# Kernel tuning notes

Measured on AMD Instinct MI355X. Metric: run time of the kernel, lower is better.

## Reference

```python
import jax, jax.numpy as jnp
import numpy as np

N_NODES = 51200
N_GRAPHS = 64
NODES_PER_GRAPH = 800
N_EDGES = 819200
DIM_IN = 128
DIM_HIDDEN = 64
HEADS = 3
DIM_OUT = 64


def leaky(x, slope):
    return jnp.where(x >= 0, x, slope * x)


def setup_inputs() -> dict:
    key = jax.random.key(0)
    ks = jax.random.split(key, 12)
    s = lambda fan_in: 1.0 / np.sqrt(fan_in)
    X = jax.random.normal(ks[0], (N_NODES, DIM_IN), dtype=jnp.float32)
    edge_indices = jax.random.randint(ks[1], (2, N_EDGES), 0, N_NODES, dtype=jnp.int32)
    ptr = (jnp.arange(N_GRAPHS + 1, dtype=jnp.int32) * NODES_PER_GRAPH)
    # linearSeq: Linear(dim_in, dim_hidden) + LeakyReLU
    W1 = jax.random.uniform(ks[2], (DIM_IN, DIM_HIDDEN), jnp.float32, -s(DIM_IN), s(DIM_IN))
    b1 = jax.random.uniform(ks[3], (DIM_HIDDEN,), jnp.float32, -s(DIM_IN), s(DIM_IN))
    # GATConv params: lin_src/lin_dst (no bias), att_src/att_dst, bias (concat=False -> out_channels)
    W_src = jax.random.uniform(ks[4], (DIM_HIDDEN, HEADS * DIM_HIDDEN), jnp.float32, -s(DIM_HIDDEN), s(DIM_HIDDEN))
    W_dst = jax.random.uniform(ks[5], (DIM_HIDDEN, HEADS * DIM_HIDDEN), jnp.float32, -s(DIM_HIDDEN), s(DIM_HIDDEN))
    att_src = jax.random.normal(ks[6], (HEADS, DIM_HIDDEN), dtype=jnp.float32) * 0.1
    att_dst = jax.random.normal(ks[7], (HEADS, DIM_HIDDEN), dtype=jnp.float32) * 0.1
    gat_bias = jnp.zeros((DIM_HIDDEN,), dtype=jnp.float32)
    # linear_final: Linear(2*dim_hidden, dim_out)
    Wf = jax.random.uniform(ks[8], (2 * DIM_HIDDEN, DIM_OUT), jnp.float32, -s(2 * DIM_HIDDEN), s(2 * DIM_HIDDEN))
    bf = jax.random.uniform(ks[9], (DIM_OUT,), jnp.float32, -s(2 * DIM_HIDDEN), s(2 * DIM_HIDDEN))
    return {"X": X, "W1": W1, "b1": b1, "W_src": W_src, "W_dst": W_dst,
            "att_src": att_src, "att_dst": att_dst, "gat_bias": gat_bias,
            "Wf": Wf, "bf": bf, "edge_indices": edge_indices, "ptr": ptr}


def reference(X, W1, b1, W_src, W_dst, att_src, att_dst, gat_bias, Wf, bf, edge_indices, ptr):
    N = X.shape[0]
    src, dst = edge_indices[0], edge_indices[1]  # message flows src -> dst
    # input projection
    h = leaky(X @ W1 + b1, 0.01)                                  # [N, DH]
    # GATConv (heads=3, concat=False, add_self_loops=False)
    x_src = (h @ W_src).reshape(N, HEADS, DIM_HIDDEN)             # [N, H, C]
    x_dst = (h @ W_dst).reshape(N, HEADS, DIM_HIDDEN)
    a_src = jnp.einsum('nhc,hc->nh', x_src, att_src)              # [N, H]
    a_dst = jnp.einsum('nhc,hc->nh', x_dst, att_dst)
    logits = leaky(a_src[src] + a_dst[dst], 0.2)                  # [E, H]
    # segment softmax over incoming edges of each target node
    m = jax.ops.segment_max(logits, dst, num_segments=N)          # [N, H]
    e = jnp.exp(logits - m[dst])
    denom = jax.ops.segment_sum(e, dst, num_segments=N)           # [N, H]
    attn = e / denom[dst]                                         # [E, H]
    msg = x_src[src] * attn[..., None]                            # [E, H, C]
    agg = jax.ops.segment_sum(msg, dst, num_segments=N)           # [N, H, C]
    out = agg.mean(axis=1) + gat_bias                             # concat=False -> head mean
    # final head
    cat = jnp.concatenate([h, out], axis=1)                       # [N, 2*DH]
    y = leaky(cat, 0.01) @ Wf + bf                                # [N, DO]
    # aggregate_using_ptr: mean-pool nodes per graph using CSR ptr
    node_graph = jnp.searchsorted(ptr, jnp.arange(N), side='right') - 1
    sums = jax.ops.segment_sum(y, node_graph, num_segments=ptr.shape[0] - 1)
    counts = (ptr[1:] - ptr[:-1]).astype(y.dtype)
    pooled = sums / counts[:, None]                               # [n_graphs, DO]
    return pooled, attn
```

## Files before the change

kernel.cpp:

```cpp
#include <hip/hip_runtime.h>
#include <hip/hip_bf16.h>

#define N_NODES   51200
#define N_GRAPHS  64
#define N_EDGES   819200
#define DIM_IN    128
#define DH        64
#define HEADS     3
#define DIM_OUT   64
#define CAP       96
#define NPART     8
#define PART_SZ   (N_NODES / NPART)

typedef __hip_bfloat16 bf16;
typedef short bf16x8 __attribute__((ext_vector_type(8)));
typedef float f32x4  __attribute__((ext_vector_type(4)));
typedef float f32x2  __attribute__((ext_vector_type(2)));

__device__ __forceinline__ float b2f(bf16 x) { return __bfloat162float(x); }
__device__ __forceinline__ bf16  f2b(float x) { return __float2bfloat16(x); }
__device__ __forceinline__ short f2bs(float x) { return (short)__bfloat16_as_ushort(f2b(x)); }
__device__ __forceinline__ float leaky(float x, float s) { return x >= 0.f ? x : s * x; }
__device__ __forceinline__ float ldin(const void* p, size_t i, int f32) {
    return f32 ? ((const float*)p)[i] : b2f(((const bf16*)p)[i]);
}
__device__ __forceinline__ bf16x8 ld8(const void* p, size_t i, int f32) {
    if (!f32) return *((const bf16x8*)((const short*)p + i));
    const float* f = (const float*)p + i;
    bf16x8 r;
    #pragma unroll
    for (int j = 0; j < 8; ++j) r[j] = f2bs(f[j]);
    return r;
}

__global__ __launch_bounds__(256) void detect_kernel(const unsigned short* __restrict__ Xu,
                                                     int* __restrict__ flag) {
    __shared__ int cnt;
    int tid = threadIdx.x;
    if (tid == 0) cnt = 0;
    __syncthreads();
    int local = 0;
    for (int i = tid * 2; i < 8192; i += 512) {
        unsigned e = (Xu[i] >> 7) & 0xFF;
        if (e >= 110 && e <= 135) local++;
    }
    atomicAdd(&cnt, local);
    __syncthreads();
    if (tid == 0) *flag = (cnt < 2048) ? 1 : 0;
}

__global__ __launch_bounds__(256) void scatter_prep_kernel(const int* __restrict__ src,
                                                           const int* __restrict__ dst,
                                                           int* __restrict__ cursor,
                                                           unsigned short* __restrict__ bucket,
                                                           const void* __restrict__ W1,
                                                           const void* __restrict__ Wsrc,
                                                           const void* __restrict__ Wdst,
                                                           const void* __restrict__ Wf,
                                                           const void* __restrict__ att_src,
                                                           const void* __restrict__ att_dst,
                                                           const int* __restrict__ flagp,
                                                           short* __restrict__ W1t,
                                                           short* __restrict__ Wallt,
                                                           short* __restrict__ Wft,
                                                           short* __restrict__ Wat) {
    if (blockIdx.x < NPART * (N_EDGES / 2048)) {
        const int p = blockIdx.x & (NPART - 1);
        const int slice = blockIdx.x >> 3;
        const int lo = p * PART_SZ, hi = lo + PART_SZ;
        const int base = slice * 2048 + threadIdx.x;
        #pragma unroll
        for (int t = 0; t < 8; ++t) {
            int e = base + t * 256;
            int d = dst[e];
            if (d >= lo && d < hi) {
                int pos = atomicAdd(&cursor[d], 1);
                if (pos < CAP) bucket[(size_t)d * CAP + pos] = (unsigned short)src[e];
            }
        }
        return;
    }
    const int f32 = *flagp;
    int idx = (blockIdx.x - NPART * (N_EDGES / 2048)) * 256 + threadIdx.x;
    if (idx < 8192) {
        int n = idx >> 7, k = idx & 127;
        W1t[idx] = f2bs(ldin(W1, (size_t)k * 64 + n, f32));
    } else if (idx < 8192 + 12288) {
        int j = idx - 8192;
        int n = j >> 6, k = j & 63;
        Wallt[j] = f2bs(ldin(Wsrc, (size_t)k * 192 + n, f32));
    } else if (idx < 8192 + 12288 + 8192) {
        int j = idx - 20480;
        int n = j >> 7, k = j & 127;
        Wft[j] = f2bs(ldin(Wf, (size_t)k * 64 + n, f32));
    } else if (idx < 8192 + 12288 + 8192 + 1024) {
        int j = idx - 28672;
        int n = j >> 6, k = j & 63;
        float v = 0.f;
        if (n < 3) {
            for (int c = 0; c < 64; ++c)
                v += ldin(Wsrc, (size_t)k * 192 + n * 64 + c, f32) * ldin(att_src, n * 64 + c, f32);
        } else if (n < 6) {
            for (int c = 0; c < 64; ++c)
                v += ldin(Wdst, (size_t)k * 192 + (n - 3) * 64 + c, f32) * ldin(att_dst, (n - 3) * 64 + c, f32);
        }
        Wat[j] = f2bs(v);
    }
}

__global__ __launch_bounds__(64) void k1_kernel(const void* __restrict__ X,
                                                const short* __restrict__ W1t,
                                                const short* __restrict__ Wallt,
                                                const short* __restrict__ Wat,
                                                const void* __restrict__ b1,
                                                const int* __restrict__ flagp,
                                                bf16* __restrict__ h_bf,
                                                unsigned* __restrict__ x8,
                                                float* __restrict__ a_src4,
                                                float* __restrict__ a_dst4) {
    const int f32 = *flagp;
    __shared__ short hs[16 * 72];
    const int lane = threadIdx.x & 63;
    const int lm   = lane & 15;
    const int q    = lane >> 4;
    const int row0 = blockIdx.x * 16;

    #pragma unroll
    for (int ct = 0; ct < 4; ++ct) {
        f32x4 acc = {0.f, 0.f, 0.f, 0.f};
        #pragma unroll
        for (int kc = 0; kc < 4; ++kc) {
            bf16x8 a = ld8(X, (size_t)(row0 + lm) * 128 + kc * 32 + q * 8, f32);
            bf16x8 b = *((const bf16x8*)(W1t + (size_t)(ct * 16 + lm) * 128 + kc * 32 + q * 8));
            acc = __builtin_amdgcn_mfma_f32_16x16x32_bf16(a, b, acc, 0, 0, 0);
        }
        const float bias = ldin(b1, ct * 16 + lm, f32);
        #pragma unroll
        for (int r = 0; r < 4; ++r) {
            int rl = q * 4 + r;
            float v = leaky(acc[r] + bias, 0.01f);
            short hv = f2bs(v);
            hs[rl * 72 + ct * 16 + lm] = hv;
            h_bf[(size_t)(row0 + rl) * 64 + ct * 16 + lm] = __ushort_as_bfloat16((unsigned short)hv);
        }
    }
    asm volatile("s_waitcnt lgkmcnt(0)" ::: "memory");

    bf16x8 a0 = *((const bf16x8*)(hs + lm * 72 + q * 8));
    bf16x8 a1 = *((const bf16x8*)(hs + lm * 72 + 32 + q * 8));
    #pragma unroll
    for (int t = 0; t < 4; ++t) {
        f32x4 acc[3];
        #pragma unroll
        for (int hh = 0; hh < 3; ++hh) {
            acc[hh] = (f32x4){0.f, 0.f, 0.f, 0.f};
            bf16x8 b0 = *((const bf16x8*)(Wallt + (size_t)(hh * 64 + t * 16 + lm) * 64 + q * 8));
            bf16x8 b1v = *((const bf16x8*)(Wallt + (size_t)(hh * 64 + t * 16 + lm) * 64 + 32 + q * 8));
            acc[hh] = __builtin_amdgcn_mfma_f32_16x16x32_bf16(a0, b0, acc[hh], 0, 0, 0);
            acc[hh] = __builtin_amdgcn_mfma_f32_16x16x32_bf16(a1, b1v, acc[hh], 0, 0, 0);
        }
        #pragma unroll
        for (int r = 0; r < 4; ++r) {
            int row = row0 + q * 4 + r;
            unsigned p = (unsigned)__builtin_amdgcn_cvt_pk_fp8_f32(acc[0][r], acc[1][r], 0, false);
            p = (unsigned)__builtin_amdgcn_cvt_pk_fp8_f32(acc[2][r], 0.f, (int)p, true);
            x8[(size_t)row * 64 + t * 16 + lm] = p;
        }
    }
    f32x4 acca = {0.f, 0.f, 0.f, 0.f};
    bf16x8 b0 = *((const bf16x8*)(Wat + (size_t)lm * 64 + q * 8));
    bf16x8 b1v = *((const bf16x8*)(Wat + (size_t)lm * 64 + 32 + q * 8));
    acca = __builtin_amdgcn_mfma_f32_16x16x32_bf16(a0, b0, acca, 0, 0, 0);
    acca = __builtin_amdgcn_mfma_f32_16x16x32_bf16(a1, b1v, acca, 0, 0, 0);
    if (lm < 6) {
        #pragma unroll
        for (int r = 0; r < 4; ++r) {
            int row = row0 + q * 4 + r;
            if (lm < 3) a_src4[(size_t)row * 4 + lm] = acca[r];
            else        a_dst4[(size_t)row * 4 + (lm - 3)] = acca[r];
        }
    }
}

__global__ __launch_bounds__(256) void edge_kernel(const unsigned short* __restrict__ bucket,
                                                   const int* __restrict__ cursor,
                                                   const float* __restrict__ a_src4,
                                                   const float* __restrict__ a_dst4,
                                                   const unsigned* __restrict__ x8,
                                                   const void* __restrict__ gat_bias,
                                                   const int* __restrict__ flagp,
                                                   float4* __restrict__ dstinfo,
                                                   bf16* __restrict__ out_agg) {
    const int f32 = *flagp;
    const int lane = threadIdx.x & 63;
    const int w = threadIdx.x >> 6;
    const int n = blockIdx.x * 4 + w;
    const int dg = min(cursor[n], CAP);
    const float4 ad = ((const float4*)a_dst4)[n];
    __shared__ float4 buf[4][64];
    float den0 = 0.f, den1 = 0.f, den2 = 0.f;
    float acc0 = 0.f, acc1 = 0.f, acc2 = 0.f;
    for (int c0 = 0; c0 < dg; c0 += 64) {
        int cnt = min(64, dg - c0);
        if (lane < cnt) {
            int s = bucket[(size_t)n * CAP + c0 + lane];
            const float4 as = ((const float4*)a_src4)[s];
            float e0 = __expf(leaky(as.x + ad.x, 0.2f));
            float e1 = __expf(leaky(as.y + ad.y, 0.2f));
            float e2 = __expf(leaky(as.z + ad.z, 0.2f));
            buf[w][lane] = make_float4(e0, e1, e2, __int_as_float(s));
        }
        asm volatile("s_waitcnt lgkmcnt(0)" ::: "memory");
        int j = 0;
        for (; j + 8 <= cnt; j += 8) {
            float4 r[8]; int xv[8];
            #pragma unroll
            for (int u = 0; u < 8; ++u) r[u] = buf[w][j + u];
            #pragma unroll
            for (int u = 0; u < 8; ++u)
                xv[u] = (int)x8[(size_t)__float_as_int(r[u].w) * 64 + lane];
            #pragma unroll
            for (int u = 0; u < 8; ++u) {
                f32x2 p = __builtin_amdgcn_cvt_pk_f32_fp8(xv[u], false);
                acc0 += r[u].x * p[0];
                acc1 += r[u].y * p[1];
                acc2 += r[u].z * __builtin_amdgcn_cvt_f32_fp8(xv[u], 2);
                den0 += r[u].x; den1 += r[u].y; den2 += r[u].z;
            }
        }
        for (; j < cnt; ++j) {
            float4 r = buf[w][j];
            int xv = (int)x8[(size_t)__float_as_int(r.w) * 64 + lane];
            f32x2 p = __builtin_amdgcn_cvt_pk_f32_fp8(xv, false);
            acc0 += r.x * p[0];
            acc1 += r.y * p[1];
            acc2 += r.z * __builtin_amdgcn_cvt_f32_fp8(xv, 2);
            den0 += r.x; den1 += r.y; den2 += r.z;
        }
    }
    float inv0 = den0 > 0.f ? 1.f / den0 : 0.f;
    float inv1 = den1 > 0.f ? 1.f / den1 : 0.f;
    float inv2 = den2 > 0.f ? 1.f / den2 : 0.f;
    float outv = (acc0 * inv0 + acc1 * inv1 + acc2 * inv2) * (1.f / 3.f) + ldin(gat_bias, lane, f32);
    out_agg[(size_t)n * DH + lane] = f2b(outv);
    if (lane == 0) {
        dstinfo[(size_t)n * 2 + 0] = make_float4(ad.x, ad.y, ad.z, 0.f);
        dstinfo[(size_t)n * 2 + 1] = make_float4(inv0, inv1, inv2, 0.f);
    }
}

__global__ __launch_bounds__(256) void attn_g3_kernel(const int* __restrict__ src,
                                                      const int* __restrict__ dst,
                                                      const float* __restrict__ a_src4,
                                                      const float4* __restrict__ dstinfo,
                                                      const bf16* __restrict__ h_bf,
                                                      const bf16* __restrict__ out_agg,
                                                      const short* __restrict__ Wft,
                                                      const void* __restrict__ bfv,
                                                      const int* __restrict__ flagp,
                                                      bf16* __restrict__ y_bf,
                                                      void* __restrict__ d_out) {
    const int f32 = *flagp;
    __shared__ short cs[64 * 136];
    if (blockIdx.x < N_EDGES / 256) {
        int e = blockIdx.x * 256 + threadIdx.x;
        int s = src[e], d = dst[e];
        const float4 as = ((const float4*)a_src4)[s];
        const float4 ad = dstinfo[(size_t)d * 2 + 0];
        const float4 cv = dstinfo[(size_t)d * 2 + 1];
        float a0 = __expf(leaky(as.x + ad.x, 0.2f)) * cv.x;
        float a1 = __expf(leaky(as.y + ad.y, 0.2f)) * cv.y;
        float a2 = __expf(leaky(as.z + ad.z, 0.2f)) * cv.z;
        size_t o = (size_t)N_GRAPHS * DIM_OUT + (size_t)e * 3;
        if (f32) {
            float* p = (float*)d_out;
            p[o] = a0; p[o + 1] = a1; p[o + 2] = a2;
        } else {
            bf16* p = (bf16*)d_out;
            p[o] = f2b(a0); p[o + 1] = f2b(a1); p[o + 2] = f2b(a2);
        }
        return;
    }
    const int bid  = blockIdx.x - N_EDGES / 256;
    const int tid  = threadIdx.x;
    const int w    = tid >> 6;
    const int lane = tid & 63;
    const int lm   = lane & 15;
    const int q    = lane >> 4;
    const int row0 = bid * 64;
    for (int idx = tid; idx < 64 * 64; idx += 256) {
        int r = idx >> 6, k = idx & 63;
        cs[r * 136 + k] = f2bs(leaky(b2f(h_bf[(size_t)(row0 + r) * 64 + k]), 0.01f));
    }
    for (int idx = tid; idx < 64 * 64; idx += 256) {
        int r = idx >> 6, k = idx & 63;
        cs[r * 136 + 64 + k] = f2bs(leaky(b2f(out_agg[(size_t)(row0 + r) * 64 + k]), 0.01f));
    }
    __syncthreads();
    const float bias = ldin(bfv, w * 16 + lm, f32);
    for (int mt = 0; mt < 4; ++mt) {
        f32x4 acc = {0.f, 0.f, 0.f, 0.f};
        #pragma unroll
        for (int kc = 0; kc < 4; ++kc) {
            bf16x8 a = *((const bf16x8*)(cs + (mt * 16 + lm) * 136 + kc * 32 + q * 8));
            bf16x8 b = *((const bf16x8*)(Wft + (size_t)(w * 16 + lm) * 128 + kc * 32 + q * 8));
            acc = __builtin_amdgcn_mfma_f32_16x16x32_bf16(a, b, acc, 0, 0, 0);
        }
        #pragma unroll
        for (int r = 0; r < 4; ++r) {
            int row = row0 + mt * 16 + q * 4 + r;
            y_bf[(size_t)row * 64 + w * 16 + lm] = f2b(acc[r] + bias);
        }
    }
}

__global__ __launch_bounds__(1024) void pool_kernel(const bf16* __restrict__ y_bf,
                                                    const int* __restrict__ ptr,
                                                    const int* __restrict__ flagp,
                                                    void* __restrict__ d_out) {
    __shared__ float part[16][64];
    const int f32 = *flagp;
    const int g = blockIdx.x;
    const int w = threadIdx.x >> 6, lane = threadIdx.x & 63;
    const int lo = ptr[g], hi = ptr[g + 1];
    const int cnt = hi - lo;
    float s = 0.f;
    for (int i = lo + w; i < hi; i += 16) s += b2f(y_bf[(size_t)i * DIM_OUT + lane]);
    part[w][lane] = s;
    __syncthreads();
    if (threadIdx.x < 64) {
        float t = 0.f;
        #pragma unroll
        for (int k = 0; k < 16; ++k) t += part[k][threadIdx.x];
        float v = t / (float)cnt;
        if (f32) ((float*)d_out)[g * DIM_OUT + threadIdx.x] = v;
        else     ((bf16*)d_out)[g * DIM_OUT + threadIdx.x]  = f2b(v);
    }
}

extern "C" void kernel_launch(void* const* d_in, const int* in_sizes, int n_in,
                              void* d_out, int out_size, void* d_ws, size_t ws_size,
                              hipStream_t stream) {
    const void* X        = d_in[0];
    const void* W1       = d_in[1];
    const void* b1       = d_in[2];
    const void* Wsrc     = d_in[3];
    const void* Wdst     = d_in[4];
    const void* att_src  = d_in[5];
    const void* att_dst  = d_in[6];
    const void* gat_bias = d_in[7];
    const void* Wf       = d_in[8];
    const void* bfv      = d_in[9];
    const int*  ei       = (const int*)d_in[10];
    const int*  ptr      = (const int*)d_in[11];
    const int*  src  = ei;
    const int*  dstp = ei + N_EDGES;

    char* ws = (char*)d_ws;
    size_t off_b = 0;
    auto alloc = [&](size_t bytes) -> char* {
        char* p = ws + off_b;
        off_b += (bytes + 255) & ~(size_t)255;
        return p;
    };
    int*     flag    = (int*)    alloc(256);
    short*   W1t     = (short*)  alloc(8192 * 2);
    short*   Wallt   = (short*)  alloc(12288 * 2);
    short*   Wft     = (short*)  alloc(8192 * 2);
    short*   Wat     = (short*)  alloc(1024 * 2);
    bf16*    h_bf    = (bf16*)   alloc((size_t)N_NODES * 64 * 2);
    unsigned* x8     = (unsigned*)alloc((size_t)N_NODES * 64 * 4);
    float*   a_src4  = (float*)  alloc((size_t)N_NODES * 16);
    float*   a_dst4  = (float*)  alloc((size_t)N_NODES * 16);
    float4*  dstinfo = (float4*) alloc((size_t)N_NODES * 2 * 16);
    bf16*    out_agg = (bf16*)   alloc((size_t)N_NODES * 64 * 2);
    int*     cursor  = (int*)    alloc((size_t)N_NODES * 4);
    unsigned short* bucket = (unsigned short*)alloc((size_t)N_NODES * CAP * 2);
    bf16*    y_bf    = (bf16*)   x8;
    if (off_b > ws_size) return;

    hipLaunchKernelGGL(detect_kernel, dim3(1), dim3(256), 0, stream,
                       (const unsigned short*)X, flag);
    hipMemsetAsync(cursor, 0, (size_t)N_NODES * 4, stream);
    hipLaunchKernelGGL(scatter_prep_kernel,
                       dim3(NPART * (N_EDGES / 2048) + 116), dim3(256), 0, stream,
                       src, dstp, cursor, bucket,
                       W1, Wsrc, Wdst, Wf, att_src, att_dst, flag, W1t, Wallt, Wft, Wat);
    hipLaunchKernelGGL(k1_kernel, dim3(N_NODES / 16), dim3(64), 0, stream,
                       X, W1t, Wallt, Wat, b1, flag, h_bf, x8, a_src4, a_dst4);
    hipLaunchKernelGGL(edge_kernel, dim3(N_NODES / 4), dim3(256), 0, stream,
                       bucket, cursor, a_src4, a_dst4, x8, gat_bias, flag, dstinfo, out_agg);
    hipLaunchKernelGGL(attn_g3_kernel, dim3(N_EDGES / 256 + N_NODES / 64), dim3(256), 0, stream,
                       src, dstp, a_src4, dstinfo, h_bf, out_agg, Wft, bfv, flag, y_bf, d_out);
    hipLaunchKernelGGL(pool_kernel, dim3(N_GRAPHS), dim3(1024), 0, stream, y_bf, ptr, flag, d_out);
}
```

Before: 247.5 us.

## Fold dtype detection into prep kernel and split fp8 head features into planes

Removes the separate single-block detect kernel: each prep block now recomputes the dtype flag locally, and one block writes it for later kernels. The per-node fp8 head features, previously packed as 4 bytes per element with one byte wasted, become three separate byte planes. The planes cut gather traffic in the edge kernel from 4 bytes to 3 bytes per element. In exchange the edge kernel issues three byte loads per gathered neighbour instead of one dword load, which may raise instruction count and memory transactions.

```diff
diff --git a/kernel.cpp b/kernel.cpp
--- a/kernel.cpp
+++ b/kernel.cpp
@@ -11,6 +11,7 @@
 #define CAP       96
 #define NPART     8
 #define PART_SZ   (N_NODES / NPART)
+#define NSCAT     (NPART * (N_EDGES / 2048))
 
 typedef __hip_bfloat16 bf16;
 typedef short bf16x8 __attribute__((ext_vector_type(8)));
@@ -33,8 +34,38 @@
     return r;
 }
 
-__global__ __launch_bounds__(256) void detect_kernel(const unsigned short* __restrict__ Xu,
-                                                     int* __restrict__ flag) {
+__global__ __launch_bounds__(256) void scatter_prep_kernel(const int* __restrict__ src,
+                                                           const int* __restrict__ dst,
+                                                           int* __restrict__ cursor,
+                                                           unsigned short* __restrict__ bucket,
+                                                           const unsigned short* __restrict__ Xu,
+                                                           const void* __restrict__ W1,
+                                                           const void* __restrict__ Wsrc,
+                                                           const void* __restrict__ Wdst,
+                                                           const void* __restrict__ Wf,
+                                                           const void* __restrict__ att_src,
+                                                           const void* __restrict__ att_dst,
+                                                           int* __restrict__ flag,
+                                                           short* __restrict__ W1t,
+                                                           short* __restrict__ Wallt,
+                                                           short* __restrict__ Wft,
+                                                           short* __restrict__ Wat) {
+    if (blockIdx.x < NSCAT) {
+        const int p = blockIdx.x & (NPART - 1);
+        const int slice = blockIdx.x >> 3;
+        const int lo = p * PART_SZ, hi = lo + PART_SZ;
+        const int base = slice * 2048 + threadIdx.x;
+        #pragma unroll
+        for (int t = 0; t < 8; ++t) {
+            int e = base + t * 256;
+            int d = dst[e];
+            if (d >= lo && d < hi) {
+                int pos = atomicAdd(&cursor[d], 1);
+                if (pos < CAP) bucket[(size_t)d * CAP + pos] = (unsigned short)src[e];
+            }
+        }
+        return;
+    }
     __shared__ int cnt;
     int tid = threadIdx.x;
     if (tid == 0) cnt = 0;
@@ -46,42 +77,10 @@
     }
     atomicAdd(&cnt, local);
     __syncthreads();
-    if (tid == 0) *flag = (cnt < 2048) ? 1 : 0;
-}
-
-__global__ __launch_bounds__(256) void scatter_prep_kernel(const int* __restrict__ src,
-                                                           const int* __restrict__ dst,
-                                                           int* __restrict__ cursor,
-                                                           unsigned short* __restrict__ bucket,
-                                                           const void* __restrict__ W1,
-                                                           const void* __restrict__ Wsrc,
-                                                           const void* __restrict__ Wdst,
-                                                           const void* __restrict__ Wf,
-                                                           const void* __restrict__ att_src,
-                                                           const void* __restrict__ att_dst,
-                                                           const int* __restrict__ flagp,
-                                                           short* __restrict__ W1t,
-                                                           short* __restrict__ Wallt,
-                                                           short* __restrict__ Wft,
-                                                           short* __restrict__ Wat) {
-    if (blockIdx.x < NPART * (N_EDGES / 2048)) {
-        const int p = blockIdx.x & (NPART - 1);
-        const int slice = blockIdx.x >> 3;
-        const int lo = p * PART_SZ, hi = lo + PART_SZ;
-        const int base = slice * 2048 + threadIdx.x;
-        #pragma unroll
-        for (int t = 0; t < 8; ++t) {
-            int e = base + t * 256;
-            int d = dst[e];
-            if (d >= lo && d < hi) {
-                int pos = atomicAdd(&cursor[d], 1);
-                if (pos < CAP) bucket[(size_t)d * CAP + pos] = (unsigned short)src[e];
-            }
-        }
-        return;
-    }
-    const int f32 = *flagp;
-    int idx = (blockIdx.x - NPART * (N_EDGES / 2048)) * 256 + threadIdx.x;
+    const int f32 = (cnt < 2048) ? 1 : 0;
+    if (blockIdx.x == NSCAT && tid == 0) *flag = f32;
+
+    int idx = (blockIdx.x - NSCAT) * 256 + tid;
     if (idx < 8192) {
         int n = idx >> 7, k = idx & 127;
         W1t[idx] = f2bs(ldin(W1, (size_t)k * 64 + n, f32));
@@ -115,7 +114,9 @@
                                                 const void* __restrict__ b1,
                                                 const int* __restrict__ flagp,
                                                 bf16* __restrict__ h_bf,
-                                                unsigned* __restrict__ x8,
+                                                unsigned char* __restrict__ xa,
+                                                unsigned char* __restrict__ xb,
+                                                unsigned char* __restrict__ xc,
                                                 float* __restrict__ a_src4,
                                                 float* __restrict__ a_dst4) {
     const int f32 = *flagp;
@@ -161,10 +162,12 @@
         }
         #pragma unroll
         for (int r = 0; r < 4; ++r) {
-            int row = row0 + q * 4 + r;
-            unsigned p = (unsigned)__builtin_amdgcn_cvt_pk_fp8_f32(acc[0][r], acc[1][r], 0, false);
-            p = (unsigned)__builtin_amdgcn_cvt_pk_fp8_f32(acc[2][r], 0.f, (int)p, true);
-            x8[(size_t)row * 64 + t * 16 + lm] = p;
+            size_t o = (size_t)(row0 + q * 4 + r) * 64 + t * 16 + lm;
+            unsigned p01 = (unsigned)__builtin_amdgcn_cvt_pk_fp8_f32(acc[0][r], acc[1][r], 0, false);
+            unsigned p2  = (unsigned)__builtin_amdgcn_cvt_pk_fp8_f32(acc[2][r], 0.f, 0, false);
+            xa[o] = (unsigned char)(p01 & 0xFFu);
+            xb[o] = (unsigned char)((p01 >> 8) & 0xFFu);
+            xc[o] = (unsigned char)(p2 & 0xFFu);
         }
     }
     f32x4 acca = {0.f, 0.f, 0.f, 0.f};
@@ -186,7 +189,9 @@
                                                    const int* __restrict__ cursor,
                                                    const float* __restrict__ a_src4,
                                                    const float* __restrict__ a_dst4,
-                                                   const unsigned* __restrict__ x8,
+                                                   const unsigned char* __restrict__ xa,
+                                                   const unsigned char* __restrict__ xb,
+                                                   const unsigned char* __restrict__ xc,
                                                    const void* __restrict__ gat_bias,
                                                    const int* __restrict__ flagp,
                                                    float4* __restrict__ dstinfo,
@@ -213,28 +218,28 @@
         asm volatile("s_waitcnt lgkmcnt(0)" ::: "memory");
         int j = 0;
         for (; j + 8 <= cnt; j += 8) {
-            float4 r[8]; int xv[8];
+            float4 r[8]; int b0[8], b1[8], b2[8];
             #pragma unroll
             for (int u = 0; u < 8; ++u) r[u] = buf[w][j + u];
             #pragma unroll
-            for (int u = 0; u < 8; ++u)
-                xv[u] = (int)x8[(size_t)__float_as_int(r[u].w) * 64 + lane];
+            for (int u = 0; u < 8; ++u) {
+                size_t o = (size_t)__float_as_int(r[u].w) * 64 + lane;
+                b0[u] = xa[o]; b1[u] = xb[o]; b2[u] = xc[o];
+            }
             #pragma unroll
             for (int u = 0; u < 8; ++u) {
-                f32x2 p = __builtin_amdgcn_cvt_pk_f32_fp8(xv[u], false);
-                acc0 += r[u].x * p[0];
-                acc1 += r[u].y * p[1];
-                acc2 += r[u].z * __builtin_amdgcn_cvt_f32_fp8(xv[u], 2);
+                acc0 += r[u].x * __builtin_amdgcn_cvt_f32_fp8(b0[u], 0);
+                acc1 += r[u].y * __builtin_amdgcn_cvt_f32_fp8(b1[u], 0);
+                acc2 += r[u].z * __builtin_amdgcn_cvt_f32_fp8(b2[u], 0);
                 den0 += r[u].x; den1 += r[u].y; den2 += r[u].z;
             }
         }
         for (; j < cnt; ++j) {
             float4 r = buf[w][j];
-            int xv = (int)x8[(size_t)__float_as_int(r.w) * 64 + lane];
-            f32x2 p = __builtin_amdgcn_cvt_pk_f32_fp8(xv, false);
-            acc0 += r.x * p[0];
-            acc1 += r.y * p[1];
-            acc2 += r.z * __builtin_amdgcn_cvt_f32_fp8(xv, 2);
+            size_t o = (size_t)__float_as_int(r.w) * 64 + lane;
+            acc0 += r.x * __builtin_amdgcn_cvt_f32_fp8((int)xa[o], 0);
+            acc1 += r.y * __builtin_amdgcn_cvt_f32_fp8((int)xb[o], 0);
+            acc2 += r.z * __builtin_amdgcn_cvt_f32_fp8((int)xc[o], 0);
             den0 += r.x; den1 += r.y; den2 += r.z;
         }
     }
@@ -369,27 +374,27 @@
     short*   Wft     = (short*)  alloc(8192 * 2);
     short*   Wat     = (short*)  alloc(1024 * 2);
     bf16*    h_bf    = (bf16*)   alloc((size_t)N_NODES * 64 * 2);
-    unsigned* x8     = (unsigned*)alloc((size_t)N_NODES * 64 * 4);
+    unsigned char* xa = (unsigned char*)alloc((size_t)N_NODES * 64);
+    unsigned char* xb = (unsigned char*)alloc((size_t)N_NODES * 64);
+    unsigned char* xc = (unsigned char*)alloc((size_t)N_NODES * 64);
     float*   a_src4  = (float*)  alloc((size_t)N_NODES * 16);
     float*   a_dst4  = (float*)  alloc((size_t)N_NODES * 16);
     float4*  dstinfo = (float4*) alloc((size_t)N_NODES * 2 * 16);
     bf16*    out_agg = (bf16*)   alloc((size_t)N_NODES * 64 * 2);
     int*     cursor  = (int*)    alloc((size_t)N_NODES * 4);
     unsigned short* bucket = (unsigned short*)alloc((size_t)N_NODES * CAP * 2);
-    bf16*    y_bf    = (bf16*)   x8;
+    bf16*    y_bf    = (bf16*)   xa;
     if (off_b > ws_size) return;
 
-    hipLaunchKernelGGL(detect_kernel, dim3(1), dim3(256), 0, stream,
-                       (const unsigned short*)X, flag);
     hipMemsetAsync(cursor, 0, (size_t)N_NODES * 4, stream);
-    hipLaunchKernelGGL(scatter_prep_kernel,
-                       dim3(NPART * (N_EDGES / 2048) + 116), dim3(256), 0, stream,
-                       src, dstp, cursor, bucket,
+    hipLaunchKernelGGL(scatter_prep_kernel, dim3(NSCAT + 116), dim3(256), 0, stream,
+                       src, dstp, cursor, bucket, (const unsigned short*)X,
                        W1, Wsrc, Wdst, Wf, att_src, att_dst, flag, W1t, Wallt, Wft, Wat);
     hipLaunchKernelGGL(k1_kernel, dim3(N_NODES / 16), dim3(64), 0, stream,
-                       X, W1t, Wallt, Wat, b1, flag, h_bf, x8, a_src4, a_dst4);
+                       X, W1t, Wallt, Wat, b1, flag, h_bf, xa, xb, xc, a_src4, a_dst4);
     hipLaunchKernelGGL(edge_kernel, dim3(N_NODES / 4), dim3(256), 0, stream,
-                       bucket, cursor, a_src4, a_dst4, x8, gat_bias, flag, dstinfo, out_agg);
+                       bucket, cursor, a_src4, a_dst4, xa, xb, xc, gat_bias, flag,
+                       dstinfo, out_agg);
     hipLaunchKernelGGL(attn_g3_kernel, dim3(N_EDGES / 256 + N_NODES / 64), dim3(256), 0, stream,
                        src, dstp, a_src4, dstinfo, h_bf, out_agg, Wft, bfv, flag, y_bf, d_out);
     hipLaunchKernelGGL(pool_kernel, dim3(N_GRAPHS), dim3(1024), 0, stream, y_bf, ptr, flag, d_out);
```

Measured after the change: 260.0 us. 1.05x slower.
